# Optimization experiments

Measured on AMD Instinct MI355X. Metric: run time of the kernel, lower is better.

The kernel has to match this reference:

```python
import jax, jax.numpy as jnp
import numpy as np

N, H, C = 1024, 128, 7

def _linear_params(key, din, dout):
    k1, k2 = jax.random.split(key)
    bound = 1.0 / np.sqrt(din)
    W = jax.random.uniform(k1, (din, dout), minval=-bound, maxval=bound, dtype=jnp.float32)
    b = jax.random.uniform(k2, (dout,), minval=-bound, maxval=bound, dtype=jnp.float32)
    return W, b

def setup_inputs() -> dict:
    key = jax.random.key(0)
    ks = jax.random.split(key, 6)
    e = jax.random.normal(ks[0], (N, H), dtype=jnp.float32)
    c = jax.random.uniform(ks[1], (N, N, C), dtype=jnp.float32)
    mW1, mb1 = _linear_params(ks[2], 2 * H + C, H)
    mW2, mb2 = _linear_params(ks[3], H, H)
    uW1, ub1 = _linear_params(ks[4], 2 * H, H)
    uW2, ub2 = _linear_params(ks[5], H, H)
    return {"e": e, "c": c,
            "mW1": mW1, "mb1": mb1, "mW2": mW2, "mb2": mb2,
            "uW1": uW1, "ub1": ub1, "uW2": uW2, "ub2": ub2}

def reference(e, c, mW1, mb1, mW2, mb2, uW1, ub1, uW2, ub2):
    n = e.shape[0]
    # z[i,j] = concat(e[i], e[j], c[i,j])  -> [N, N, 2H+C]
    x = jnp.broadcast_to(e[:, None, :], (n, n, H))  # sender rows
    y = jnp.broadcast_to(e[None, :, :], (n, n, H))  # receiver cols
    z = jnp.concatenate([x, y, c], axis=2)
    h = jax.nn.relu(jnp.einsum('ijk,kh->ijh', z, mW1) + mb1)
    m = jnp.einsum('ijh,hk->ijk', h, mW2) + mb2
    agg = m.sum(axis=1)  # [N, H]
    u = jnp.concatenate([agg, e], axis=1)  # [N, 2H]
    out = jax.nn.relu(u @ uW1 + ub1) @ uW2 + ub2
    return out
```

## Files before the change

### kernel.cpp

```cpp
#include <hip/hip_runtime.h>

#define NN 1024
#define HH 128
#define CC 7
#define BI 8
#define BJ 64
#define NCH 4
#define NSLICE 16
#define QPADU 68

typedef __attribute__((ext_vector_type(8))) short bf16x8;
typedef __attribute__((ext_vector_type(4))) float f32x4;

__device__ inline unsigned f2bf(float x) {
    union { float f; unsigned u; } v; v.f = x;
    return (v.u + 0x7FFFu + ((v.u >> 16) & 1u)) >> 16;
}
__device__ inline unsigned bfrnd(unsigned u) {
    return u + 0x7FFFu + ((u >> 16) & 1u);
}
__device__ inline float bitsf(unsigned u) {
    union { unsigned u; float f; } v; v.u = u; return v.f;
}

__global__ __launch_bounds__(256) void precompute_pq(
    const float* __restrict__ e, const float* __restrict__ mW1,
    const float* __restrict__ mb1, float* __restrict__ P, unsigned* __restrict__ Qpk)
{
    const int t  = threadIdx.x;
    const int rr = t >> 7;
    const int h  = t & 127;
    const int i0 = blockIdx.x * 2;
    __shared__ float eL[2][HH];
    __shared__ float qs[2][HH];
    eL[rr][h] = e[(size_t)(i0 + rr) * HH + h];
    __syncthreads();
    float p = mb1[h], q = 0.f;
    for (int k = 0; k < HH; ++k) {
        const float ev = eL[rr][k];
        p = fmaf(ev, mW1[k * HH + h], p);
        q = fmaf(ev, mW1[(HH + k) * HH + h], q);
    }
    P[(size_t)(i0 + rr) * HH + h] = p;
    qs[rr][h] = q;
    __syncthreads();
    if (h < 64) {
        const unsigned lo = f2bf(qs[rr][h]);
        const unsigned hi = f2bf(qs[rr][h + 64]);
        Qpk[(size_t)(i0 + rr) * 64 + h] = lo | (hi << 16);
    }
}

__global__ __launch_bounds__(256, 5) void msg_mfma(
    const float* __restrict__ c, const float* __restrict__ mW1,
    const float* __restrict__ P, const unsigned* __restrict__ Qpk,
    float* __restrict__ HSp)
{
    const int bid   = blockIdx.x;
    const int islab = bid >> 4;
    const int slice = bid & 15;
    const int i0    = islab * BI;
    const int j0b   = slice * BJ;
    const int t     = threadIdx.x;
    const int w     = t >> 6;
    const int l     = t & 63;
    const int g     = l >> 4;
    const int col   = l & 15;
    const int iw0   = i0 + 2 * w;

    __shared__ unsigned qpk[BJ * QPADU];
    __shared__ uint4 abuf[BI * BJ];
    __shared__ uint4 bld[129];
    __shared__ float pld[BI * HH];

    #pragma unroll
    for (int rep = 0; rep < 4; ++rep) {
        const int idx = t + rep * 256;
        const int row = idx >> 4;
        const int c4  = (idx & 15) * 4;
        *(uint4*)(qpk + row * QPADU + c4) =
            *(const uint4*)(Qpk + (size_t)(j0b + row) * 64 + c4);
    }
    #pragma unroll
    for (int rep = 0; rep < 2; ++rep) {
        const int rr = t + rep * 256;
        const int ii = rr >> 6;
        const int jj = rr & 63;
        const unsigned* __restrict__ cp = (const unsigned*)
            (c + ((size_t)(i0 + ii) * NN + j0b + jj) * CC);
        unsigned d0 = bfrnd(cp[0]), d1 = bfrnd(cp[1]), d2 = bfrnd(cp[2]);
        unsigned d3 = bfrnd(cp[3]), d4 = bfrnd(cp[4]), d5 = bfrnd(cp[5]);
        unsigned d6 = bfrnd(cp[6]);
        uint4 pk;
        pk.x = __builtin_amdgcn_perm(d1, d0, 0x07060302u);
        pk.y = __builtin_amdgcn_perm(d3, d2, 0x07060302u);
        pk.z = __builtin_amdgcn_perm(d5, d4, 0x07060302u);
        pk.w = d6 >> 16;
        abuf[rr] = pk;
    }
    if (t < 128) {
        const int ht = t >> 4;
        const int cl = t & 15;
        const float* __restrict__ wp = mW1 + (2 * HH) * HH + 16 * ht + cl;
        uint4 bv;
        bv.x = f2bf(wp[0])      | (f2bf(wp[HH])     << 16);
        bv.y = f2bf(wp[2 * HH]) | (f2bf(wp[3 * HH]) << 16);
        bv.z = f2bf(wp[4 * HH]) | (f2bf(wp[5 * HH]) << 16);
        bv.w = f2bf(wp[6 * HH]);
        bld[t] = bv;
    } else if (t == 128) {
        bld[128] = (uint4){0u, 0u, 0u, 0u};
    }
    #pragma unroll
    for (int rep = 0; rep < 4; ++rep) {
        const int idx = t + rep * 256;
        pld[idx] = P[(size_t)i0 * HH + idx];
    }

    float acc[2][8];
    #pragma unroll
    for (int ii = 0; ii < 2; ++ii)
        #pragma unroll
        for (int ht = 0; ht < 8; ++ht) acc[ii][ht] = 0.f;

    __syncthreads();

    bf16x8 af[2][NCH];
    #pragma unroll
    for (int ch = 0; ch < NCH; ++ch) {
        af[0][ch] = __builtin_bit_cast(bf16x8, abuf[(2 * w + 0) * 64 + ch * 16 + col]);
        af[1][ch] = __builtin_bit_cast(bf16x8, abuf[(2 * w + 1) * 64 + ch * 16 + col]);
    }

    const int pbase0 = (2 * w + 0) * HH + col;
    const int pbase1 = (2 * w + 1) * HH + col;

    #pragma unroll 1
    for (int hp = 0; hp < 4; ++hp) {
        const int bi_lo = (g == 0) ? (hp * 16 + col) : 128;
        const int bi_hi = (g == 0) ? ((hp + 4) * 16 + col) : 128;
        const bf16x8 blo = __builtin_bit_cast(bf16x8, bld[bi_lo]);
        const bf16x8 bhi = __builtin_bit_cast(bf16x8, bld[bi_hi]);
        const float pv0lo = pld[pbase0 + 16 * hp];
        const float pv1lo = pld[pbase1 + 16 * hp];
        const float pv0hi = pld[pbase0 + 16 * (hp + 4)];
        const float pv1hi = pld[pbase1 + 16 * (hp + 4)];
        #pragma unroll
        for (int ch = 0; ch < NCH; ++ch) {
            unsigned u[4];
            #pragma unroll
            for (int r = 0; r < 4; ++r)
                u[r] = qpk[(ch * 16 + g * 4 + r) * QPADU + 16 * hp + col];
            {
                f32x4 d0, d1;
                #pragma unroll
                for (int r = 0; r < 4; ++r) {
                    const float fa = bitsf(u[r] << 16);
                    d0[r] = pv0lo + fa;
                    d1[r] = pv1lo + fa;
                }
                d0 = __builtin_amdgcn_mfma_f32_16x16x32_bf16(af[0][ch], blo, d0, 0, 0, 0);
                d1 = __builtin_amdgcn_mfma_f32_16x16x32_bf16(af[1][ch], blo, d1, 0, 0, 0);
                #pragma unroll
                for (int r = 0; r < 4; ++r) {
                    acc[0][hp] += fmaxf(d0[r], 0.f);
                    acc[1][hp] += fmaxf(d1[r], 0.f);
                }
            }
            {
                f32x4 d0, d1;
                #pragma unroll
                for (int r = 0; r < 4; ++r) {
                    const float fb = bitsf(u[r] & 0xFFFF0000u);
                    d0[r] = pv0hi + fb;
                    d1[r] = pv1hi + fb;
                }
                d0 = __builtin_amdgcn_mfma_f32_16x16x32_bf16(af[0][ch], bhi, d0, 0, 0, 0);
                d1 = __builtin_amdgcn_mfma_f32_16x16x32_bf16(af[1][ch], bhi, d1, 0, 0, 0);
                #pragma unroll
                for (int r = 0; r < 4; ++r) {
                    acc[0][hp + 4] += fmaxf(d0[r], 0.f);
                    acc[1][hp + 4] += fmaxf(d1[r], 0.f);
                }
            }
        }
    }

    #pragma unroll
    for (int ii = 0; ii < 2; ++ii)
        #pragma unroll
        for (int ht = 0; ht < 8; ++ht) {
            float a = acc[ii][ht];
            a += __shfl_xor(a, 16, 64);
            a += __shfl_xor(a, 32, 64);
            acc[ii][ht] = a;
        }
    #pragma unroll
    for (int ii = 0; ii < 2; ++ii)
        #pragma unroll
        for (int s = 0; s < 2; ++s) {
            const int ht = g + 4 * s;
            HSp[((size_t)slice * NN + iw0 + ii) * HH + 16 * ht + col] = acc[ii][ht];
        }
}

__global__ __launch_bounds__(256) void final_mlp(
    const float* __restrict__ e, const float* __restrict__ HSp,
    const float* __restrict__ mW2, const float* __restrict__ mb2,
    const float* __restrict__ uW1, const float* __restrict__ ub1,
    const float* __restrict__ uW2, const float* __restrict__ ub2,
    float* __restrict__ out)
{
    const int t  = threadIdx.x;
    const int s  = t >> 7;
    const int h  = t & 127;
    const int i0 = blockIdx.x * 2;
    __shared__ float hsL[2][HH], eL[2][HH], aggL[2][HH], t1L[2][HH], part[2][2][HH];

    {
        const size_t ih = (size_t)(i0 + s) * HH + h;
        float sum = 0.f;
        #pragma unroll
        for (int sl = 0; sl < NSLICE; ++sl)
            sum += HSp[(size_t)sl * NN * HH + ih];
        hsL[s][h] = sum;
        eL[s][h]  = e[ih];
    }
    __syncthreads();

    {
        float a0 = 0.f, a1 = 0.f;
        const int k0 = 64 * s;
        for (int k = k0; k < k0 + 64; ++k) {
            const float wv = mW2[k * HH + h];
            a0 = fmaf(hsL[0][k], wv, a0);
            a1 = fmaf(hsL[1][k], wv, a1);
        }
        part[s][0][h] = a0; part[s][1][h] = a1;
    }
    __syncthreads();
    aggL[s][h] = part[0][s][h] + part[1][s][h] + (float)NN * mb2[h];
    __syncthreads();

    {
        float b0 = 0.f, b1 = 0.f;
        const float* __restrict__ src   = (s == 0) ? &aggL[0][0] : &eL[0][0];
        const float* __restrict__ wbase = uW1 + (size_t)s * HH * HH;
        for (int k = 0; k < HH; ++k) {
            const float wv = wbase[k * HH + h];
            b0 = fmaf(src[k],      wv, b0);
            b1 = fmaf(src[HH + k], wv, b1);
        }
        part[s][0][h] = b0; part[s][1][h] = b1;
    }
    __syncthreads();
    t1L[s][h] = fmaxf(part[0][s][h] + part[1][s][h] + ub1[h], 0.f);
    __syncthreads();

    {
        float c0 = 0.f, c1 = 0.f;
        const int k0 = 64 * s;
        for (int k = k0; k < k0 + 64; ++k) {
            const float wv = uW2[k * HH + h];
            c0 = fmaf(t1L[0][k], wv, c0);
            c1 = fmaf(t1L[1][k], wv, c1);
        }
        part[s][0][h] = c0; part[s][1][h] = c1;
    }
    __syncthreads();
    out[(size_t)(i0 + s) * HH + h] = part[0][s][h] + part[1][s][h] + ub2[h];
}

extern "C" void kernel_launch(void* const* d_in, const int* in_sizes, int n_in,
                              void* d_out, int out_size, void* d_ws, size_t ws_size,
                              hipStream_t stream) {
    const float* e   = (const float*)d_in[0];
    const float* c   = (const float*)d_in[1];
    const float* mW1 = (const float*)d_in[2];
    const float* mb1 = (const float*)d_in[3];
    const float* mW2 = (const float*)d_in[4];
    const float* mb2 = (const float*)d_in[5];
    const float* uW1 = (const float*)d_in[6];
    const float* ub1 = (const float*)d_in[7];
    const float* uW2 = (const float*)d_in[8];
    const float* ub2 = (const float*)d_in[9];
    float* out = (float*)d_out;

    float*    P   = (float*)d_ws;
    unsigned* Qpk = (unsigned*)(P + NN * HH);
    float*    HSp = (float*)(Qpk + NN * 64);

    precompute_pq<<<NN / 2, 256, 0, stream>>>(e, mW1, mb1, P, Qpk);
    msg_mfma<<<(NN / BI) * NSLICE, 256, 0, stream>>>(c, mW1, P, Qpk, HSp);
    final_mlp<<<NN / 2, 256, 0, stream>>>(e, HSp, mW2, mb2, uW1, ub1, uW2, ub2, out);
}
```

Baseline: 48.32 us.

## Reduce message partials with atomics and split precompute over K

```diff
diff --git a/kernel.cpp b/kernel.cpp
--- a/kernel.cpp
+++ b/kernel.cpp
@@ -25,36 +25,42 @@
 
 __global__ __launch_bounds__(256) void precompute_pq(
     const float* __restrict__ e, const float* __restrict__ mW1,
-    const float* __restrict__ mb1, float* __restrict__ P, unsigned* __restrict__ Qpk)
+    const float* __restrict__ mb1, float* __restrict__ P,
+    unsigned* __restrict__ Qpk, float* __restrict__ HS)
 {
-    const int t  = threadIdx.x;
-    const int rr = t >> 7;
-    const int h  = t & 127;
-    const int i0 = blockIdx.x * 2;
-    __shared__ float eL[2][HH];
-    __shared__ float qs[2][HH];
-    eL[rr][h] = e[(size_t)(i0 + rr) * HH + h];
-    __syncthreads();
-    float p = mb1[h], q = 0.f;
-    for (int k = 0; k < HH; ++k) {
-        const float ev = eL[rr][k];
+    const int row = blockIdx.x;
+    const int t   = threadIdx.x;
+    const int s   = t >> 7;
+    const int h   = t & 127;
+    __shared__ float eL[HH];
+    __shared__ float part[2][2][HH];
+    __shared__ float qs[HH];
+    if (s == 0) eL[h] = e[(size_t)row * HH + h];
+    else        HS[(size_t)row * HH + h] = 0.f;
+    __syncthreads();
+    float p = 0.f, q = 0.f;
+    const int k0 = s * 64;
+    for (int k = k0; k < k0 + 64; ++k) {
+        const float ev = eL[k];
         p = fmaf(ev, mW1[k * HH + h], p);
         q = fmaf(ev, mW1[(HH + k) * HH + h], q);
     }
-    P[(size_t)(i0 + rr) * HH + h] = p;
-    qs[rr][h] = q;
-    __syncthreads();
-    if (h < 64) {
-        const unsigned lo = f2bf(qs[rr][h]);
-        const unsigned hi = f2bf(qs[rr][h + 64]);
-        Qpk[(size_t)(i0 + rr) * 64 + h] = lo | (hi << 16);
+    part[s][0][h] = p; part[s][1][h] = q;
+    __syncthreads();
+    if (s == 0) P[(size_t)row * HH + h] = part[0][0][h] + part[1][0][h] + mb1[h];
+    else        qs[h] = part[0][1][h] + part[1][1][h];
+    __syncthreads();
+    if (t < 64) {
+        const unsigned lo = f2bf(qs[t]);
+        const unsigned hi = f2bf(qs[t + 64]);
+        Qpk[(size_t)row * 64 + t] = lo | (hi << 16);
     }
 }
 
 __global__ __launch_bounds__(256, 5) void msg_mfma(
     const float* __restrict__ c, const float* __restrict__ mW1,
     const float* __restrict__ P, const unsigned* __restrict__ Qpk,
-    float* __restrict__ HSp)
+    float* __restrict__ HS)
 {
     const int bid   = blockIdx.x;
     const int islab = bid >> 4;
@@ -200,12 +206,12 @@
         #pragma unroll
         for (int s = 0; s < 2; ++s) {
             const int ht = g + 4 * s;
-            HSp[((size_t)slice * NN + iw0 + ii) * HH + 16 * ht + col] = acc[ii][ht];
+            atomicAdd(&HS[(size_t)(iw0 + ii) * HH + 16 * ht + col], acc[ii][ht]);
         }
 }
 
 __global__ __launch_bounds__(256) void final_mlp(
-    const float* __restrict__ e, const float* __restrict__ HSp,
+    const float* __restrict__ e, const float* __restrict__ HS,
     const float* __restrict__ mW2, const float* __restrict__ mb2,
     const float* __restrict__ uW1, const float* __restrict__ ub1,
     const float* __restrict__ uW2, const float* __restrict__ ub2,
@@ -219,11 +225,7 @@
 
     {
         const size_t ih = (size_t)(i0 + s) * HH + h;
-        float sum = 0.f;
-        #pragma unroll
-        for (int sl = 0; sl < NSLICE; ++sl)
-            sum += HSp[(size_t)sl * NN * HH + ih];
-        hsL[s][h] = sum;
+        hsL[s][h] = HS[ih];
         eL[s][h]  = e[ih];
     }
     __syncthreads();
@@ -288,9 +290,9 @@
 
     float*    P   = (float*)d_ws;
     unsigned* Qpk = (unsigned*)(P + NN * HH);
-    float*    HSp = (float*)(Qpk + NN * 64);
-
-    precompute_pq<<<NN / 2, 256, 0, stream>>>(e, mW1, mb1, P, Qpk);
-    msg_mfma<<<(NN / BI) * NSLICE, 256, 0, stream>>>(c, mW1, P, Qpk, HSp);
-    final_mlp<<<NN / 2, 256, 0, stream>>>(e, HSp, mW2, mb2, uW1, ub1, uW2, ub2, out);
-}
+    float*    HS  = (float*)(Qpk + NN * 64);
+
+    precompute_pq<<<NN, 256, 0, stream>>>(e, mW1, mb1, P, Qpk, HS);
+    msg_mfma<<<(NN / BI) * NSLICE, 256, 0, stream>>>(c, mW1, P, Qpk, HS);
+    final_mlp<<<NN / 2, 256, 0, stream>>>(e, HS, mW2, mb2, uW1, ub1, uW2, ub2, out);
+}
```

New measurement: 45.82 us, median of 2. -5.2%, faster.
